# Kernel tuning notes

Hardware: AMD Instinct MI355X
Metric: run time of the kernel (lower is better)

Reference implementation:

```python
import jax, jax.numpy as jnp
import numpy as np

M_POOL = 5000  # rows of down_transform (coarse mesh size)


def setup_inputs() -> dict:
    key = jax.random.key(0)
    ks = jax.random.split(key, 6)
    bs, n_nodes, c_in, seq_len, c_out = 16, 20000, 32, 9, 64
    x = jax.random.normal(ks[0], (bs, n_nodes, c_in), dtype=jnp.float32)
    indices = jax.random.randint(ks[1], (n_nodes, seq_len), 0, n_nodes, dtype=jnp.int32)
    # xavier-uniform-ish linear weight
    fan_in, fan_out = c_in * seq_len, c_out
    limit = float(np.sqrt(6.0 / (fan_in + fan_out)))
    weight = jax.random.uniform(ks[2], (c_out, fan_in), minval=-limit, maxval=limit, dtype=jnp.float32)
    bias = jnp.zeros((c_out,), dtype=jnp.float32)
    trans_rows = jax.random.randint(ks[3], (20000,), 0, M_POOL, dtype=jnp.int32)
    trans_cols = jax.random.randint(ks[4], (20000,), 0, n_nodes, dtype=jnp.int32)
    trans_vals = jax.random.uniform(ks[5], (20000,), dtype=jnp.float32)
    return {"x": x, "indices": indices, "weight": weight, "bias": bias,
            "trans_rows": trans_rows, "trans_cols": trans_cols, "trans_vals": trans_vals}


def reference(x, indices, weight, bias, trans_rows, trans_cols, trans_vals):
    bs = x.shape[0]
    n_nodes, seq_len = indices.shape
    # SpiralConv: gather spiral neighborhoods -> [bs, n_nodes, seq_len*c_in]
    g = x[:, indices.reshape(-1), :].reshape(bs, n_nodes, -1)
    h = jnp.einsum('bnk,ok->bno', g, weight) + bias  # [bs, n_nodes, c_out]
    h = jax.nn.elu(h)
    # Pool: sparse down_transform @ h  (scatter_add over COO entries)
    contrib = h[:, trans_cols, :] * trans_vals[None, :, None]  # [bs, nnz, c_out]
    out = jnp.zeros((bs, M_POOL, h.shape[-1]), dtype=h.dtype)
    out = out.at[:, trans_rows, :].add(contrib)
    return out
```

## Files before the change

### kernel.cpp

```cpp
#include <hip/hip_runtime.h>

#define BS 16
#define NNODES 20000
#define CIN 32
#define SEQ 9
#define COUT 64
#define KTOT 288
#define MPOOL 5000
#define NNZ 20000

#define H_BYTES   40960000ULL
#define XB_BYTES  20480000ULL
#define WF_BYTES  36864ULL
#define CV_BYTES  (NNZ * 8ULL)
#define START_BYTES ((MPOOL + 1) * 4ULL)
#define CNTCUR_BYTES (2ULL * MPOOL * 4ULL)

#define XBLK (NNODES / 4)
#define WBLK 9
#define ZBLK 10

typedef __attribute__((ext_vector_type(8))) short bf16x8;
typedef __attribute__((ext_vector_type(4))) float f32x4;

static __device__ __forceinline__ unsigned short f2bf(float f) {
  unsigned u = __float_as_uint(f);
  u += 0x7FFF + ((u >> 16) & 1);
  return (unsigned short)(u >> 16);
}
static __device__ __forceinline__ float bf2f(short s) {
  return __uint_as_float(((unsigned)(unsigned short)s) << 16);
}
static __device__ __forceinline__ unsigned cvt_pk_bf16(float lo, float hi) {
  unsigned r;
  asm("v_cvt_pk_bf16_f32 %0, %1, %2" : "=v"(r) : "v"(lo), "v"(hi));
  return r;
}

__global__ __launch_bounds__(256) void prep_kernel(const float* __restrict__ x,
                                                   const float* __restrict__ weight,
                                                   unsigned short* __restrict__ xbT,
                                                   unsigned short* __restrict__ wf,
                                                   int* __restrict__ cntcur) {
  const int id = blockIdx.x;
  if (id < XBLK) {
    const int wv = threadIdx.x >> 6, lane = threadIdx.x & 63;
    const int n = id * 4 + wv;
    const int b = lane >> 2, c8 = (lane & 3) * 8;
    const float* src = x + ((size_t)b * NNODES + n) * CIN + c8;
    const float4 u0 = ((const float4*)src)[0];
    const float4 u1 = ((const float4*)src)[1];
    uint4 p;
    p.x = (unsigned)f2bf(u0.x) | ((unsigned)f2bf(u0.y) << 16);
    p.y = (unsigned)f2bf(u0.z) | ((unsigned)f2bf(u0.w) << 16);
    p.z = (unsigned)f2bf(u1.x) | ((unsigned)f2bf(u1.y) << 16);
    p.w = (unsigned)f2bf(u1.z) | ((unsigned)f2bf(u1.w) << 16);
    *(uint4*)&xbT[(size_t)n * 512 + (size_t)lane * 8] = p;
  } else if (id < XBLK + WBLK) {
    const int t = (id - XBLK) * 256 + threadIdx.x;
    if (t < SEQ * 4 * 64) {
      const int f0 = t * 8;
      const int blk = f0 >> 9;
      const int inb = f0 & 511;
      const int lhi = inb >> 7;
      const int l16 = (inb >> 3) & 15;
      const int kk = blk >> 2, o = blk & 3;
      const float* src = weight + (size_t)(o * 16 + l16) * KTOT + kk * 32 + lhi * 8;
      const float4 u0 = ((const float4*)src)[0];
      const float4 u1 = ((const float4*)src)[1];
      uint4 p;
      p.x = (unsigned)f2bf(u0.x) | ((unsigned)f2bf(u0.y) << 16);
      p.y = (unsigned)f2bf(u0.z) | ((unsigned)f2bf(u0.w) << 16);
      p.z = (unsigned)f2bf(u1.x) | ((unsigned)f2bf(u1.y) << 16);
      p.w = (unsigned)f2bf(u1.z) | ((unsigned)f2bf(u1.w) << 16);
      *(uint4*)&wf[f0] = p;
    }
  } else {
    const int base = (id - XBLK - WBLK) * 1024 + threadIdx.x;
#pragma unroll
    for (int j = 0; j < 4; ++j) {
      const int i = base + j * 256;
      if (i < 2 * MPOOL) cntcur[i] = 0;
    }
  }
}

__global__ __launch_bounds__(256) void hist_kernel(const int* __restrict__ rows,
                                                   int* __restrict__ cnt) {
  const int k = blockIdx.x * 256 + threadIdx.x;
  if (k < NNZ) atomicAdd(&cnt[rows[k]], 1);
}

__global__ __launch_bounds__(256) void scan_kernel(const int* __restrict__ cnt,
                                                   int* __restrict__ start) {
  __shared__ int part[256];
  const int t = threadIdx.x;
  const int base = t * 20;
  int local[20];
  int s = 0;
#pragma unroll
  for (int j = 0; j < 20; ++j) {
    const int i = base + j;
    local[j] = s;
    s += (i < MPOOL) ? cnt[i] : 0;
  }
  part[t] = s;
  __syncthreads();
  for (int off = 1; off < 256; off <<= 1) {
    const int v = (t >= off) ? part[t - off] : 0;
    __syncthreads();
    part[t] += v;
    __syncthreads();
  }
  const int excl = (t == 0) ? 0 : part[t - 1];
#pragma unroll
  for (int j = 0; j < 20; ++j) {
    const int i = base + j;
    if (i < MPOOL) start[i] = excl + local[j];
  }
  if (t == 255) start[MPOOL] = NNZ;
}

__global__ __launch_bounds__(256) void reorder_kernel(const int* __restrict__ rows,
                                                      const int* __restrict__ cols,
                                                      const float* __restrict__ vals,
                                                      const int* __restrict__ start,
                                                      int* __restrict__ cursor,
                                                      int2* __restrict__ cvp) {
  const int k = blockIdx.x * 256 + threadIdx.x;
  if (k < NNZ) {
    const int r = rows[k];
    const int pos = start[r] + atomicAdd(&cursor[r], 1);
    cvp[pos] = make_int2(cols[k], __float_as_int(vals[k]));
  }
}

__global__ __launch_bounds__(512, 8) void gemm_elu_kernel(
    const unsigned short* __restrict__ xbT,
    const int* __restrict__ indices,
    const unsigned short* __restrict__ wf,
    const float* __restrict__ bias,
    unsigned short* __restrict__ hT)
{
  __shared__ unsigned short wlds[SEQ * 4 * 512];

  const int tid = threadIdx.x;
  {
    const uint4* src = (const uint4*)wf;
    uint4* dst = (uint4*)wlds;
    for (int i = tid; i < (SEQ * 4 * 512) / 8; i += 512) dst[i] = src[i];
  }
  __syncthreads();

  const int wv = __builtin_amdgcn_readfirstlane(tid >> 6);
  const int lane = tid & 63;
  const int l16 = lane & 15;
  const int lhi = lane >> 4;
  const int n = blockIdx.x * 8 + wv;

  const int aoff = l16 * 32 + lhi * 8;
  const int boff = lane * 8;

  int gi[SEQ];
  {
    const int* __restrict__ ip = indices + (size_t)n * SEQ;
#pragma unroll
    for (int kk = 0; kk < SEQ; ++kk) gi[kk] = ip[kk];
  }

  f32x4 acc[4];
#pragma unroll
  for (int o = 0; o < 4; ++o) {
    f32x4 z = {0.f, 0.f, 0.f, 0.f};
    acc[o] = z;
  }

#pragma unroll
  for (int kk = 0; kk < SEQ; ++kk) {
    const bf16x8 af = *(const bf16x8*)&xbT[(size_t)gi[kk] * 512 + aoff];
    const bf16x8 b0 = *(const bf16x8*)&wlds[(kk * 4 + 0) * 512 + boff];
    const bf16x8 b1 = *(const bf16x8*)&wlds[(kk * 4 + 1) * 512 + boff];
    const bf16x8 b2 = *(const bf16x8*)&wlds[(kk * 4 + 2) * 512 + boff];
    const bf16x8 b3 = *(const bf16x8*)&wlds[(kk * 4 + 3) * 512 + boff];
    acc[0] = __builtin_amdgcn_mfma_f32_16x16x32_bf16(af, b0, acc[0], 0, 0, 0);
    acc[1] = __builtin_amdgcn_mfma_f32_16x16x32_bf16(af, b1, acc[1], 0, 0, 0);
    acc[2] = __builtin_amdgcn_mfma_f32_16x16x32_bf16(af, b2, acc[2], 0, 0, 0);
    acc[3] = __builtin_amdgcn_mfma_f32_16x16x32_bf16(af, b3, acc[3], 0, 0, 0);
  }

#pragma unroll
  for (int o = 0; o < 4; ++o) {
    const int oc = o * 16 + l16;
    const float bv = bias[oc];
    float v0 = acc[o][0] + bv, v1 = acc[o][1] + bv;
    float v2 = acc[o][2] + bv, v3 = acc[o][3] + bv;
    v0 = v0 > 0.f ? v0 : (__expf(v0) - 1.f);
    v1 = v1 > 0.f ? v1 : (__expf(v1) - 1.f);
    v2 = v2 > 0.f ? v2 : (__expf(v2) - 1.f);
    v3 = v3 > 0.f ? v3 : (__expf(v3) - 1.f);
    uint2 p;
    p.x = cvt_pk_bf16(v0, v1);
    p.y = cvt_pk_bf16(v2, v3);
    *(uint2*)&hT[(size_t)n * 1024 + oc * 16 + lhi * 4] = p;
  }
}

__global__ __launch_bounds__(256) void pool_kernel(
    const unsigned short* __restrict__ hT,
    const int* __restrict__ start,
    const int2* __restrict__ cvp,
    float* __restrict__ out)
{
  const int r = blockIdx.x * 4 + (threadIdx.x >> 6);
  const int lane = threadIdx.x & 63;

  float acc[16];
#pragma unroll
  for (int b = 0; b < 16; ++b) acc[b] = 0.f;

  const int s = start[r], e = start[r + 1];
  int2 cv = (s < e) ? cvp[s] : make_int2(0, 0);
  for (int j = s; j < e; ++j) {
    const int2 cvn = (j + 1 < e) ? cvp[j + 1] : make_int2(0, 0);
    const int c = cv.x;
    const float v = __int_as_float(cv.y);
    const unsigned short* hp = hT + (size_t)c * 1024 + lane * 16;
    const bf16x8 h0 = *(const bf16x8*)hp;
    const bf16x8 h1 = *(const bf16x8*)(hp + 8);
#pragma unroll
    for (int b = 0; b < 8; ++b) {
      acc[b]     += v * bf2f(h0[b]);
      acc[b + 8] += v * bf2f(h1[b]);
    }
    cv = cvn;
  }
#pragma unroll
  for (int b = 0; b < 16; ++b)
    out[((size_t)b * MPOOL + r) * COUT + lane] = acc[b];
}

__global__ __launch_bounds__(256) void scatter_kernel(
    const unsigned short* __restrict__ hT,
    const int* __restrict__ rows,
    const int* __restrict__ cols,
    const float* __restrict__ vals,
    float* __restrict__ out)
{
  const int gw = (int)((blockIdx.x * blockDim.x + threadIdx.x) >> 6);
  const int lane = threadIdx.x & 63;
  const int nw = (int)((gridDim.x * blockDim.x) >> 6);
  for (int t = gw; t < NNZ * BS; t += nw) {
    const int k = t >> 4;
    const int b = t & 15;
    const float hv = bf2f((short)hT[(size_t)cols[k] * 1024 + lane * 16 + b]);
    atomicAdd(&out[((size_t)b * MPOOL + rows[k]) * COUT + lane], hv * vals[k]);
  }
}

extern "C" void kernel_launch(void* const* d_in, const int* in_sizes, int n_in,
                              void* d_out, int out_size, void* d_ws, size_t ws_size,
                              hipStream_t stream) {
  const float* x       = (const float*)d_in[0];
  const int*   indices = (const int*)d_in[1];
  const float* weight  = (const float*)d_in[2];
  const float* bias    = (const float*)d_in[3];
  const int*   trows   = (const int*)d_in[4];
  const int*   tcols   = (const int*)d_in[5];
  const float* tvals   = (const float*)d_in[6];
  float* out = (float*)d_out;

  char* w = (char*)d_ws;
  unsigned short* hT  = (unsigned short*)w;
  unsigned short* xbT = (unsigned short*)(w + H_BYTES);
  unsigned short* wf  = (unsigned short*)(w + H_BYTES + XB_BYTES);
  int2* cvp  = (int2*)(w + H_BYTES + XB_BYTES + WF_BYTES);
  int* start = (int*)(w + H_BYTES + XB_BYTES + WF_BYTES + CV_BYTES);
  int* cnt   = (int*)(w + H_BYTES + XB_BYTES + WF_BYTES + CV_BYTES + START_BYTES);
  int* cursor = cnt + MPOOL;

  const bool big_ws = (ws_size >=
      H_BYTES + XB_BYTES + WF_BYTES + CV_BYTES + START_BYTES + CNTCUR_BYTES);

  prep_kernel<<<XBLK + WBLK + ZBLK, 256, 0, stream>>>(x, weight, xbT, wf, cnt);

  if (big_ws) {
    hist_kernel<<<(NNZ + 255) / 256, 256, 0, stream>>>(trows, cnt);
    scan_kernel<<<1, 256, 0, stream>>>(cnt, start);
    reorder_kernel<<<(NNZ + 255) / 256, 256, 0, stream>>>(trows, tcols, tvals,
                                                          start, cursor, cvp);
  }

  gemm_elu_kernel<<<NNODES / 8, 512, 0, stream>>>(xbT, indices, wf, bias, hT);

  if (big_ws) {
    pool_kernel<<<MPOOL / 4, 256, 0, stream>>>(hT, start, cvp, out);
  } else {
    hipMemsetAsync(d_out, 0, (size_t)out_size * sizeof(float), stream);
    scatter_kernel<<<4096, 256, 0, stream>>>(hT, trows, tcols, tvals, out);
  }
}
```

Before: 70.64 us.

## Reorganize activations into batch-pair groups so each MFMA tile spans 8 nodes

Changes the bf16 x and h layouts from node-major with all 16 batches interleaved to 8 groups of batch pairs, each stored as [node][64]. The GEMM now assigns each wave 8 nodes × 2 batches per 16-row MFMA tile, stages the spiral indices in LDS, and splits the grid by batch group. The aim is to improve locality in the gather: each gathered row is 128 bytes per group rather than a 1 KB node row read piecemeal. The pool kernel now reads 8 separate strided 4-byte loads per nonzero instead of two contiguous 16-byte loads, which could cost more in that stage.

```diff
diff --git a/kernel.cpp b/kernel.cpp
--- a/kernel.cpp
+++ b/kernel.cpp
@@ -28,8 +28,8 @@
   u += 0x7FFF + ((u >> 16) & 1);
   return (unsigned short)(u >> 16);
 }
-static __device__ __forceinline__ float bf2f(short s) {
-  return __uint_as_float(((unsigned)(unsigned short)s) << 16);
+static __device__ __forceinline__ float bf2f(unsigned short s) {
+  return __uint_as_float(((unsigned)s) << 16);
 }
 static __device__ __forceinline__ unsigned cvt_pk_bf16(float lo, float hi) {
   unsigned r;
@@ -39,14 +39,17 @@
 
 __global__ __launch_bounds__(256) void prep_kernel(const float* __restrict__ x,
                                                    const float* __restrict__ weight,
-                                                   unsigned short* __restrict__ xbT,
+                                                   unsigned short* __restrict__ xbT2,
                                                    unsigned short* __restrict__ wf,
                                                    int* __restrict__ cntcur) {
   const int id = blockIdx.x;
   if (id < XBLK) {
-    const int wv = threadIdx.x >> 6, lane = threadIdx.x & 63;
-    const int n = id * 4 + wv;
-    const int b = lane >> 2, c8 = (lane & 3) * 8;
+    const int W = id * 4 + (threadIdx.x >> 6);
+    const int lane = threadIdx.x & 63;
+    const unsigned b = (unsigned)W / 1250u;
+    const unsigned tile = (unsigned)W % 1250u;
+    const int n = (int)tile * 16 + (lane >> 2);
+    const int c8 = (lane & 3) * 8;
     const float* src = x + ((size_t)b * NNODES + n) * CIN + c8;
     const float4 u0 = ((const float4*)src)[0];
     const float4 u1 = ((const float4*)src)[1];
@@ -55,7 +58,8 @@
     p.y = (unsigned)f2bf(u0.z) | ((unsigned)f2bf(u0.w) << 16);
     p.z = (unsigned)f2bf(u1.x) | ((unsigned)f2bf(u1.y) << 16);
     p.w = (unsigned)f2bf(u1.z) | ((unsigned)f2bf(u1.w) << 16);
-    *(uint4*)&xbT[(size_t)n * 512 + (size_t)lane * 8] = p;
+    const int g = (int)(b >> 1), bl = (int)(b & 1);
+    *(uint4*)&xbT2[((size_t)g * NNODES + n) * 64 + bl * 32 + c8] = p;
   } else if (id < XBLK + WBLK) {
     const int t = (id - XBLK) * 256 + threadIdx.x;
     if (t < SEQ * 4 * 64) {
@@ -136,37 +140,42 @@
 }
 
 __global__ __launch_bounds__(512, 8) void gemm_elu_kernel(
-    const unsigned short* __restrict__ xbT,
+    const unsigned short* __restrict__ xbT2,
     const int* __restrict__ indices,
     const unsigned short* __restrict__ wf,
     const float* __restrict__ bias,
-    unsigned short* __restrict__ hT)
+    unsigned* __restrict__ hT)
 {
   __shared__ unsigned short wlds[SEQ * 4 * 512];
+  __shared__ int idx_lds[64 * SEQ];
 
   const int tid = threadIdx.x;
+  const int g = blockIdx.x & 7;
+  const int n0 = (blockIdx.x >> 3) * 64;
+
   {
     const uint4* src = (const uint4*)wf;
     uint4* dst = (uint4*)wlds;
-    for (int i = tid; i < (SEQ * 4 * 512) / 8; i += 512) dst[i] = src[i];
+    for (int i = tid; i < (SEQ * 4 * 512 * 2) / 16; i += 512)
+      dst[i] = src[i];
+  }
+  for (int i = tid; i < 64 * SEQ; i += 512) {
+    const int gidx = n0 * SEQ + i;
+    idx_lds[i] = (gidx < NNODES * SEQ) ? indices[gidx] : 0;
   }
   __syncthreads();
 
-  const int wv = __builtin_amdgcn_readfirstlane(tid >> 6);
+  const int wv = tid >> 6;
   const int lane = tid & 63;
   const int l16 = lane & 15;
   const int lhi = lane >> 4;
-  const int n = blockIdx.x * 8 + wv;
-
-  const int aoff = l16 * 32 + lhi * 8;
+  const int n0w = n0 + wv * 8;
+  if (n0w >= NNODES) return;
+
+  const unsigned short* __restrict__ xg = xbT2 + (size_t)g * NNODES * 64;
+  const int moff = (l16 & 1) * 32 + lhi * 8;
   const int boff = lane * 8;
-
-  int gi[SEQ];
-  {
-    const int* __restrict__ ip = indices + (size_t)n * SEQ;
-#pragma unroll
-    for (int kk = 0; kk < SEQ; ++kk) gi[kk] = ip[kk];
-  }
+  const int idxbase = (wv * 8 + (l16 >> 1)) * SEQ;
 
   f32x4 acc[4];
 #pragma unroll
@@ -177,7 +186,8 @@
 
 #pragma unroll
   for (int kk = 0; kk < SEQ; ++kk) {
-    const bf16x8 af = *(const bf16x8*)&xbT[(size_t)gi[kk] * 512 + aoff];
+    const int gi = idx_lds[idxbase + kk];
+    const bf16x8 af = *(const bf16x8*)&xg[(size_t)gi * 64 + moff];
     const bf16x8 b0 = *(const bf16x8*)&wlds[(kk * 4 + 0) * 512 + boff];
     const bf16x8 b1 = *(const bf16x8*)&wlds[(kk * 4 + 1) * 512 + boff];
     const bf16x8 b2 = *(const bf16x8*)&wlds[(kk * 4 + 2) * 512 + boff];
@@ -188,6 +198,8 @@
     acc[3] = __builtin_amdgcn_mfma_f32_16x16x32_bf16(af, b3, acc[3], 0, 0, 0);
   }
 
+  unsigned* __restrict__ hg = hT + (size_t)g * NNODES * 64;
+  const int nA = n0w + lhi * 2;
 #pragma unroll
   for (int o = 0; o < 4; ++o) {
     const int oc = o * 16 + l16;
@@ -198,15 +210,13 @@
     v1 = v1 > 0.f ? v1 : (__expf(v1) - 1.f);
     v2 = v2 > 0.f ? v2 : (__expf(v2) - 1.f);
     v3 = v3 > 0.f ? v3 : (__expf(v3) - 1.f);
-    uint2 p;
-    p.x = cvt_pk_bf16(v0, v1);
-    p.y = cvt_pk_bf16(v2, v3);
-    *(uint2*)&hT[(size_t)n * 1024 + oc * 16 + lhi * 4] = p;
+    hg[(size_t)nA * 64 + oc]       = cvt_pk_bf16(v0, v1);
+    hg[(size_t)(nA + 1) * 64 + oc] = cvt_pk_bf16(v2, v3);
   }
 }
 
 __global__ __launch_bounds__(256) void pool_kernel(
-    const unsigned short* __restrict__ hT,
+    const unsigned* __restrict__ hT,
     const int* __restrict__ start,
     const int2* __restrict__ cvp,
     float* __restrict__ out)
@@ -224,13 +234,11 @@
     const int2 cvn = (j + 1 < e) ? cvp[j + 1] : make_int2(0, 0);
     const int c = cv.x;
     const float v = __int_as_float(cv.y);
-    const unsigned short* hp = hT + (size_t)c * 1024 + lane * 16;
-    const bf16x8 h0 = *(const bf16x8*)hp;
-    const bf16x8 h1 = *(const bf16x8*)(hp + 8);
-#pragma unroll
-    for (int b = 0; b < 8; ++b) {
-      acc[b]     += v * bf2f(h0[b]);
-      acc[b + 8] += v * bf2f(h1[b]);
+#pragma unroll
+    for (int g = 0; g < 8; ++g) {
+      const unsigned u = hT[((size_t)g * NNODES + c) * 64 + lane];
+      acc[2 * g]     += v * bf2f((unsigned short)(u & 0xffff));
+      acc[2 * g + 1] += v * bf2f((unsigned short)(u >> 16));
     }
     cv = cvn;
   }
@@ -240,7 +248,7 @@
 }
 
 __global__ __launch_bounds__(256) void scatter_kernel(
-    const unsigned short* __restrict__ hT,
+    const unsigned* __restrict__ hT,
     const int* __restrict__ rows,
     const int* __restrict__ cols,
     const float* __restrict__ vals,
@@ -252,7 +260,8 @@
   for (int t = gw; t < NNZ * BS; t += nw) {
     const int k = t >> 4;
     const int b = t & 15;
-    const float hv = bf2f((short)hT[(size_t)cols[k] * 1024 + lane * 16 + b]);
+    const unsigned u = hT[((size_t)(b >> 1) * NNODES + cols[k]) * 64 + lane];
+    const float hv = bf2f((unsigned short)((b & 1) ? (u >> 16) : (u & 0xffff)));
     atomicAdd(&out[((size_t)b * MPOOL + rows[k]) * COUT + lane], hv * vals[k]);
   }
 }
@@ -270,9 +279,9 @@
   float* out = (float*)d_out;
 
   char* w = (char*)d_ws;
-  unsigned short* hT  = (unsigned short*)w;
-  unsigned short* xbT = (unsigned short*)(w + H_BYTES);
-  unsigned short* wf  = (unsigned short*)(w + H_BYTES + XB_BYTES);
+  unsigned* hT         = (unsigned*)w;
+  unsigned short* xbT2 = (unsigned short*)(w + H_BYTES);
+  unsigned short* wf   = (unsigned short*)(w + H_BYTES + XB_BYTES);
   int2* cvp  = (int2*)(w + H_BYTES + XB_BYTES + WF_BYTES);
   int* start = (int*)(w + H_BYTES + XB_BYTES + WF_BYTES + CV_BYTES);
   int* cnt   = (int*)(w + H_BYTES + XB_BYTES + WF_BYTES + CV_BYTES + START_BYTES);
@@ -281,7 +290,7 @@
   const bool big_ws = (ws_size >=
       H_BYTES + XB_BYTES + WF_BYTES + CV_BYTES + START_BYTES + CNTCUR_BYTES);
 
-  prep_kernel<<<XBLK + WBLK + ZBLK, 256, 0, stream>>>(x, weight, xbT, wf, cnt);
+  prep_kernel<<<XBLK + WBLK + ZBLK, 256, 0, stream>>>(x, weight, xbT2, wf, cnt);
 
   if (big_ws) {
     hist_kernel<<<(NNZ + 255) / 256, 256, 0, stream>>>(trows, cnt);
@@ -290,7 +299,7 @@
                                                           start, cursor, cvp);
   }
 
-  gemm_elu_kernel<<<NNODES / 8, 512, 0, stream>>>(xbT, indices, wf, bias, hT);
+  gemm_elu_kernel<<<313 * 8, 512, 0, stream>>>(xbT2, indices, wf, bias, hT);
 
   if (big_ws) {
     pool_kernel<<<MPOOL / 4, 256, 0, stream>>>(hT, start, cvp, out);
```

New measurement: 61.49 us, median of 2. 1.15x faster.
